# Kernel tuning notes

Measured on AMD Instinct MI355X. Metric: run time of the kernel, lower is better.

The kernel has to match this reference:

```python
import jax, jax.numpy as jnp
import numpy as np


def setup_inputs() -> dict:
    key = jax.random.key(0)
    ks = jax.random.split(key, 5)
    B, C, H, W = 4, 256, 48, 48
    x = jax.random.normal(ks[0], (B, C, H, W), dtype=jnp.float32)
    w_qkv = jax.random.normal(ks[1], (3 * C, C), dtype=jnp.float32) * (C ** -0.5)
    b_qkv = jax.random.normal(ks[2], (3 * C,), dtype=jnp.float32) * 0.02
    w_proj = jax.random.normal(ks[3], (C, C), dtype=jnp.float32) * (C ** -0.5)
    b_proj = jax.random.normal(ks[4], (C,), dtype=jnp.float32) * 0.02
    return {"x": x, "w_qkv": w_qkv, "b_qkv": b_qkv, "w_proj": w_proj, "b_proj": b_proj, "num_heads": 4}


def reference(x, w_qkv, b_qkv, w_proj, b_proj, num_heads):
    B, C, H, W = x.shape
    N = H * W
    hd = C // num_heads
    # NOTE: original uses full-dim scale, not head_dim
    scale = C ** -0.5
    # 1x1 conv == channel matmul
    qkv = jnp.einsum('bchw,oc->bohw', x, w_qkv) + b_qkv[None, :, None, None]
    qkv = qkv.reshape(B, 3, num_heads, hd, N)
    q = qkv[:, 0].transpose(0, 1, 3, 2)  # [B, h, N, d]
    k = qkv[:, 1]                         # [B, h, d, N]
    v = qkv[:, 2].transpose(0, 1, 3, 2)  # [B, h, N, d]
    attn = jax.nn.softmax((q @ k) * scale, axis=-1)  # [B, h, N, N]
    out = attn @ v                        # [B, h, N, d]
    out = out.transpose(0, 1, 3, 2).reshape(B, C, H, W)
    return jnp.einsum('bchw,oc->bohw', out, w_proj) + b_proj[None, :, None, None]
```

## Files before the change

kernel.cpp:

```cpp
#include <hip/hip_runtime.h>
#include <hip/hip_bf16.h>
#include <stdint.h>

typedef unsigned short u16;
typedef unsigned int u32;
typedef __attribute__((ext_vector_type(8))) short bf16x8;
typedef __attribute__((ext_vector_type(4))) float f32x4;
typedef __attribute__((ext_vector_type(4))) unsigned short u16x4;

#define MFMA16 __builtin_amdgcn_mfma_f32_16x16x32_bf16

static constexpr int Bb = 4;
static constexpr int Cc = 256;
static constexpr int NHh = 4;
static constexpr int HDd = 64;
static constexpr int Nn = 2304;

__device__ __forceinline__ u16 f2bf(float f) {
  u32 u = __builtin_bit_cast(u32, f);
  u32 r = u + 0x7fffu + ((u >> 16) & 1u);
  return (u16)(r >> 16);
}

__device__ __forceinline__ u32 cvtpk(float a, float b) {
  u32 r;
  asm("v_cvt_pk_bf16_f32 %0, %1, %2" : "=v"(r) : "v"(a), "v"(b));
  return r;
}

__device__ __forceinline__ void async16(const void* g, void* l) {
  __builtin_amdgcn_global_load_lds(
      (const __attribute__((address_space(1))) u32*)g,
      (__attribute__((address_space(3))) u32*)l, 16, 0, 0);
}

__global__ __launch_bounds__(256) void k_prep(const float* __restrict__ wq,
                                              const float* __restrict__ wp,
                                              const float* __restrict__ x,
                                              u16* __restrict__ wqb,
                                              u16* __restrict__ wpb,
                                              u16* __restrict__ xT) {
  __shared__ float tile[64][65];
  int bx = blockIdx.x;
  if (bx < 768) {
    int i = bx * 256 + threadIdx.x;
    if (i < 3 * Cc * Cc) wqb[i] = f2bf(wq[i]);
    if (i < Cc * Cc)     wpb[i] = f2bf(wp[i]);
    return;
  }
  int t2 = bx - 768;
  int c0 = (t2 & 3) * 64, n0 = ((t2 >> 2) % 36) * 64, b = (t2 >> 2) / 36;
  int w = threadIdx.x >> 6, lane = threadIdx.x & 63;
#pragma unroll
  for (int i = 0; i < 16; ++i) {
    int c = i * 4 + w;
    tile[c][lane] = x[((size_t)(b * Cc + c0 + c)) * Nn + n0 + lane];
  }
  __syncthreads();
#pragma unroll
  for (int i = 0; i < 16; ++i) {
    int n = i * 4 + w;
    xT[((size_t)(b * Nn + n0 + n)) * Cc + c0 + lane] = f2bf(tile[lane][n]);
  }
}

__global__ __launch_bounds__(256) void k_qkv(const u16* __restrict__ wqb,
                                             const u16* __restrict__ xT,
                                             const float* __restrict__ bqkv,
                                             u16* __restrict__ qT, u16* __restrict__ kT,
                                             u16* __restrict__ vT) {
  __shared__ u16 Bs[64 * 256];
  int n0 = blockIdx.y * 64, b = blockIdx.z;
  int t = threadIdx.x, w = t >> 6, l = t & 63, g = l >> 4, li = l & 15;
#pragma unroll
  for (int it = 0; it < 8; ++it) {
    int ch = it * 256 + t;
    int row = ch >> 5, c16 = ch & 31;
    const char* src = (const char*)xT + ((size_t)(b * Nn + n0 + row)) * 512 +
                      ((c16 * 16) ^ ((row & 7) << 4));
    async16(src, (char*)Bs + (it * 256 + (t & ~63)) * 16);
  }
  __syncthreads();
  const float qs = 0.0625f * 1.44269504088896340736f;
#pragma unroll
  for (int p = 0; p < 2; ++p) {
    int o0 = blockIdx.x * 128 + p * 64;
    const u16* Arow = wqb + (size_t)(o0 + w * 16 + li) * Cc;
    f32x4 acc[4] = {};
#pragma unroll
    for (int s = 0; s < 8; ++s) {
      bf16x8 a = *(const bf16x8*)(Arow + s * 32 + g * 8);
#pragma unroll
      for (int nt = 0; nt < 4; ++nt) {
        int row = nt * 16 + li;
        const char* bp_ = (const char*)Bs + row * 512 + ((s * 64 + g * 16) ^ ((row & 7) << 4));
        bf16x8 bb = *(const bf16x8*)bp_;
        acc[nt] = MFMA16(a, bb, acc[nt], 0, 0, 0);
      }
    }
    int which = o0 >> 8;
    int hh = (o0 >> 6) & 3;
    int bh = b * NHh + hh;
    int dbase = w * 16 + g * 4;
#pragma unroll
    for (int nt = 0; nt < 4; ++nt) {
      int n = n0 + nt * 16 + li;
      float v0 = acc[nt][0] + bqkv[o0 + dbase + 0];
      float v1 = acc[nt][1] + bqkv[o0 + dbase + 1];
      float v2 = acc[nt][2] + bqkv[o0 + dbase + 2];
      float v3 = acc[nt][3] + bqkv[o0 + dbase + 3];
      if (which == 0) {
        u16x4 pq = {f2bf(v0 * qs), f2bf(v1 * qs), f2bf(v2 * qs), f2bf(v3 * qs)};
        *(u16x4*)(qT + ((size_t)bh * Nn + n) * HDd + dbase) = pq;
      } else if (which == 1) {
        u16x4 pk = {f2bf(v0), f2bf(v1), f2bf(v2), f2bf(v3)};
        *(u16x4*)(kT + ((size_t)bh * Nn + n) * HDd + dbase) = pk;
      } else {
        vT[((size_t)bh * HDd + dbase + 0) * Nn + n] = f2bf(v0);
        vT[((size_t)bh * HDd + dbase + 1) * Nn + n] = f2bf(v1);
        vT[((size_t)bh * HDd + dbase + 2) * Nn + n] = f2bf(v2);
        vT[((size_t)bh * HDd + dbase + 3) * Nn + n] = f2bf(v3);
      }
    }
  }
}

__global__ __launch_bounds__(192) void k_attn(const u16* __restrict__ qT,
                                              const u16* __restrict__ kT,
                                              const u16* __restrict__ vT,
                                              u16* __restrict__ attP,
                                              float* __restrict__ lsumP) {
  __shared__ u16 Ks[2][32 * 64];
  __shared__ u16 Vs[2][64 * 32];
  __shared__ u16 Ps[3][32 * 32];
  int L = blockIdx.x;
  int xcd = L & 7, r = L >> 3;
  int bh = 2 * xcd + (r >= 96 ? 1 : 0);
  int r2 = (r >= 96) ? r - 96 : r;
  int quarter = r2 / 24;
  int qb = r2 % 24;
  int t = threadIdx.x, w = t / 64, l = t & 63, g = l >> 4, li = l & 15;
  int q0 = qb * 96 + w * 32;
  const u16* qr0 = qT + ((size_t)bh * Nn + q0 + li) * HDd;
  const u16* qr1 = qT + ((size_t)bh * Nn + q0 + 16 + li) * HDd;
  bf16x8 bq[2][2];
  bq[0][0] = *(const bf16x8*)(qr0 + g * 8);
  bq[0][1] = *(const bf16x8*)(qr0 + 32 + g * 8);
  bq[1][0] = *(const bf16x8*)(qr1 + g * 8);
  bq[1][1] = *(const bf16x8*)(qr1 + 32 + g * 8);
  const short one = (short)0x3F80;
  bf16x8 ONES = {one, one, one, one, one, one, one, one};
  f32x4 acc[2][4] = {};
  f32x4 acc_l[2] = {};
  const char* kbh = (const char*)(kT + (size_t)bh * Nn * HDd);
  const char* vbh = (const char*)(vT + (size_t)bh * HDd * Nn);
  char* PsB = (char*)(&Ps[w][0]);
  int sw_li = (li & 7) << 4;
  int sw2   = ((li >> 1) & 3) << 4;

  const char* sp[3];
  int sd[3];
  ptrdiff_t sstr[3];
  bool son[3], svv[3];
#pragma unroll
  for (int it = 0; it < 3; ++it) {
    int gg = w * 3 + it;
    son[it] = (gg < 8);
    int c = gg * 64 + l;
    if (c < 256) {
      int key = c >> 3, c8 = c & 7;
      sp[it] = kbh + (size_t)(quarter * 576 + key) * 128 + ((c8 * 16) ^ ((key & 7) << 4));
      sd[it] = c * 16; sstr[it] = 32 * 128; svv[it] = false;
    } else {
      int cv = c - 256, d = cv >> 2, c4 = cv & 3;
      sp[it] = vbh + (size_t)d * (Nn * 2) + quarter * 1152 +
               ((c4 * 16) ^ (((d >> 1) & 3) << 4));
      sd[it] = cv * 16; sstr[it] = 32 * 2; svv[it] = true;
    }
  }

  auto STAGE = [&](int buf) {
    char* kdst = (char*)(&Ks[0][0]) + buf * 4096;
    char* vdst = (char*)(&Vs[0][0]) + buf * 4096;
#pragma unroll
    for (int it = 0; it < 3; ++it) {
      if (son[it]) {
        async16(sp[it], (svv[it] ? vdst : kdst) + sd[it]);
        sp[it] += sstr[it];
      }
    }
  };

  STAGE(0);
  int cur = 0;
  for (int kb = 0; kb < 18; ++kb) {
    __syncthreads();
    if (kb + 1 < 18) STAGE(cur ^ 1);

    const char* Kc = (const char*)(&Ks[0][0]) + cur * 4096;
    const char* Vc = (const char*)(&Vs[0][0]) + cur * 4096;

    f32x4 s[2][2];
    __builtin_amdgcn_s_setprio(1);
#pragma unroll
    for (int kt = 0; kt < 2; ++kt) {
      const char* kr = Kc + (kt * 16 + li) * 128;
      bf16x8 a0 = *(const bf16x8*)(kr + ((g * 16) ^ sw_li));
      bf16x8 a1 = *(const bf16x8*)(kr + ((64 + g * 16) ^ sw_li));
#pragma unroll
      for (int st = 0; st < 2; ++st) {
        f32x4 z = {};
        z = MFMA16(a0, bq[st][0], z, 0, 0, 0);
        z = MFMA16(a1, bq[st][1], z, 0, 0, 0);
        s[st][kt] = z;
      }
    }
    __builtin_amdgcn_s_setprio(0);

#pragma unroll
    for (int st = 0; st < 2; ++st) {
#pragma unroll
      for (int kt = 0; kt < 2; ++kt)
#pragma unroll
        for (int j = 0; j < 4; ++j) s[st][kt][j] = exp2f(s[st][kt][j]);
      int rq = st * 16 + li;
#pragma unroll
      for (int kt = 0; kt < 2; ++kt) {
        uint2 pk;
        pk.x = cvtpk(s[st][kt][0], s[st][kt][1]);
        pk.y = cvtpk(s[st][kt][2], s[st][kt][3]);
        *(uint2*)(PsB + rq * 64 + ((kt * 32 + g * 8) ^ sw2)) = pk;
      }
    }
    bf16x8 pa[2];
    pa[0] = *(const bf16x8*)(PsB + (0 * 16 + li) * 64 + ((g * 16) ^ sw2));
    pa[1] = *(const bf16x8*)(PsB + (1 * 16 + li) * 64 + ((g * 16) ^ sw2));
    __builtin_amdgcn_s_setprio(1);
    acc_l[0] = MFMA16(pa[0], ONES, acc_l[0], 0, 0, 0);
    acc_l[1] = MFMA16(pa[1], ONES, acc_l[1], 0, 0, 0);
#pragma unroll
    for (int dt = 0; dt < 4; ++dt) {
      const char* vr = Vc + (dt * 16 + li) * 64;
      bf16x8 v0 = *(const bf16x8*)(vr + ((g * 16) ^ sw2));
      acc[0][dt] = MFMA16(pa[0], v0, acc[0][dt], 0, 0, 0);
      acc[1][dt] = MFMA16(pa[1], v0, acc[1][dt], 0, 0, 0);
    }
    __builtin_amdgcn_s_setprio(0);
    cur ^= 1;
  }
  u16* ap = attP + (size_t)quarter * (Bb * Nn * Cc);
  float* lp = lsumP + quarter * (Bb * NHh * Nn);
  if (li == 0) {
#pragma unroll
    for (int st = 0; st < 2; ++st)
#pragma unroll
      for (int j = 0; j < 4; ++j)
        lp[bh * Nn + q0 + st * 16 + g * 4 + j] = acc_l[st][j];
  }
  int b = bh >> 2, hh = bh & 3;
#pragma unroll
  for (int st = 0; st < 2; ++st)
#pragma unroll
    for (int dt = 0; dt < 4; ++dt) {
      int cidx = hh * 64 + dt * 16 + li;
#pragma unroll
      for (int j = 0; j < 4; ++j) {
        ap[((size_t)(b * Nn + q0 + st * 16 + g * 4 + j)) * Cc + cidx] = f2bf(acc[st][dt][j]);
      }
    }
}

__global__ __launch_bounds__(256) void k_proj(const u16* __restrict__ wpb,
                                              const u16* __restrict__ attP,
                                              const float* __restrict__ lsumP,
                                              const float* __restrict__ bp,
                                              float* __restrict__ out) {
  __shared__ u16 Bs[4][32 * 256];
  int bx = blockIdx.x, n0 = blockIdx.y * 32, b = blockIdx.z;
  int t = threadIdx.x, w = t >> 6, l = t & 63, g = l >> 4, li = l & 15;
#pragma unroll
  for (int it = 0; it < 16; ++it) {
    int ch = it * 256 + t;
    int qtr = ch >> 10, rem = ch & 1023;
    int row = rem >> 5, c16 = rem & 31;
    const char* src = (const char*)(attP + (size_t)qtr * (Bb * Nn * Cc)) +
                      ((size_t)(b * Nn + n0 + row)) * 512 +
                      ((c16 * 16) ^ ((row & 7) << 4));
    async16(src, (char*)Bs + (it * 256 + (t & ~63)) * 16);
  }
  const u16* Arow0 = wpb + (size_t)(bx * 128 + w * 16 + li) * Cc;
  const u16* Arow1 = Arow0 + (size_t)64 * Cc;
  __syncthreads();
  f32x4 acc[2][4][2] = {};
#pragma unroll
  for (int s = 0; s < 8; ++s) {
    bf16x8 a0 = *(const bf16x8*)(Arow0 + s * 32 + g * 8);
    bf16x8 a1 = *(const bf16x8*)(Arow1 + s * 32 + g * 8);
#pragma unroll
    for (int qtr = 0; qtr < 4; ++qtr) {
#pragma unroll
      for (int nt = 0; nt < 2; ++nt) {
        int row = nt * 16 + li;
        const char* bp_ = (const char*)Bs + qtr * (32 * 512) + row * 512 +
                          ((s * 64 + g * 16) ^ ((row & 7) << 4));
        bf16x8 bb = *(const bf16x8*)bp_;
        acc[0][s >> 1][nt] = MFMA16(a0, bb, acc[0][s >> 1][nt], 0, 0, 0);
        acc[1][s >> 1][nt] = MFMA16(a1, bb, acc[1][s >> 1][nt], 0, 0, 0);
      }
    }
  }
#pragma unroll
  for (int nt = 0; nt < 2; ++nt) {
    int n = n0 + nt * 16 + li;
    float inv[4];
#pragma unroll
    for (int h = 0; h < 4; ++h) {
      int lidx = (b * NHh + h) * Nn + n;
      float sum = lsumP[lidx] + lsumP[1 * Bb * NHh * Nn + lidx] +
                  lsumP[2 * Bb * NHh * Nn + lidx] + lsumP[3 * Bb * NHh * Nn + lidx];
      inv[h] = 1.0f / sum;
    }
#pragma unroll
    for (int p = 0; p < 2; ++p) {
      int obase = bx * 128 + p * 64 + w * 16 + g * 4;
#pragma unroll
      for (int j = 0; j < 4; ++j) {
        float v = acc[p][0][nt][j] * inv[0] + acc[p][1][nt][j] * inv[1] +
                  acc[p][2][nt][j] * inv[2] + acc[p][3][nt][j] * inv[3];
        out[((size_t)(b * Cc + obase + j)) * Nn + n] = v + bp[obase + j];
      }
    }
  }
}

extern "C" void kernel_launch(void* const* d_in, const int* in_sizes, int n_in,
                              void* d_out, int out_size, void* d_ws, size_t ws_size,
                              hipStream_t stream) {
  const float* x     = (const float*)d_in[0];
  const float* wqkv  = (const float*)d_in[1];
  const float* bqkv  = (const float*)d_in[2];
  const float* wproj = (const float*)d_in[3];
  const float* bproj = (const float*)d_in[4];
  float* out = (float*)d_out;

  u16* ws    = (u16*)d_ws;
  u16* wq_bf = ws;
  u16* wp_bf = wq_bf + 196608;
  u16* qT    = wp_bf + 65536;
  u16* kT    = qT + 2359296;
  u16* vT    = kT + 2359296;
  u16* attP  = vT + 2359296;
  u16* xT    = attP;
  float* lsumP = (float*)(attP + 4 * 2359296);

  k_prep<<<dim3(1344), dim3(256), 0, stream>>>(wqkv, wproj, x, wq_bf, wp_bf, xT);
  k_qkv<<<dim3(6, 36, 4), dim3(256), 0, stream>>>(wq_bf, xT, bqkv, qT, kT, vT);
  k_attn<<<dim3(1536), dim3(192), 0, stream>>>(qT, kT, vT, attP, lsumP);
  k_proj<<<dim3(2, 72, 4), dim3(256), 0, stream>>>(wp_bf, attP, lsumP, bproj, out);
}
```

Measured before the change: 84.31 us.

## Fuse x transpose into QKV kernel and add split-merge kernel before projection

The x transpose/bf16 conversion moves out of the prep kernel into the QKV kernel, which now reads fp32 x directly and transposes it through LDS. This removes the xT round trip through global memory. A new merge kernel sums the four split-K partial attention outputs, normalises them by the combined softmax sums, and writes a single bf16 tensor into the qT buffer. The projection then does a quarter of its previous MFMA work and loads less data into LDS. The cost is an extra kernel launch plus a full read/write pass for the merge, and the QKV kernel now repeats the x transpose in each of its six output-channel blocks.

```diff
diff --git a/kernel.cpp b/kernel.cpp
--- a/kernel.cpp
+++ b/kernel.cpp
@@ -28,6 +28,9 @@
   return r;
 }
 
+__device__ __forceinline__ float blo(u32 u) { return __builtin_bit_cast(float, u << 16); }
+__device__ __forceinline__ float bhi(u32 u) { return __builtin_bit_cast(float, u & 0xffff0000u); }
+
 __device__ __forceinline__ void async16(const void* g, void* l) {
   __builtin_amdgcn_global_load_lds(
       (const __attribute__((address_space(1))) u32*)g,
@@ -36,51 +39,39 @@
 
 __global__ __launch_bounds__(256) void k_prep(const float* __restrict__ wq,
                                               const float* __restrict__ wp,
-                                              const float* __restrict__ x,
                                               u16* __restrict__ wqb,
-                                              u16* __restrict__ wpb,
-                                              u16* __restrict__ xT) {
-  __shared__ float tile[64][65];
-  int bx = blockIdx.x;
-  if (bx < 768) {
-    int i = bx * 256 + threadIdx.x;
-    if (i < 3 * Cc * Cc) wqb[i] = f2bf(wq[i]);
-    if (i < Cc * Cc)     wpb[i] = f2bf(wp[i]);
-    return;
-  }
-  int t2 = bx - 768;
-  int c0 = (t2 & 3) * 64, n0 = ((t2 >> 2) % 36) * 64, b = (t2 >> 2) / 36;
-  int w = threadIdx.x >> 6, lane = threadIdx.x & 63;
-#pragma unroll
-  for (int i = 0; i < 16; ++i) {
-    int c = i * 4 + w;
-    tile[c][lane] = x[((size_t)(b * Cc + c0 + c)) * Nn + n0 + lane];
-  }
-  __syncthreads();
-#pragma unroll
-  for (int i = 0; i < 16; ++i) {
-    int n = i * 4 + w;
-    xT[((size_t)(b * Nn + n0 + n)) * Cc + c0 + lane] = f2bf(tile[lane][n]);
-  }
+                                              u16* __restrict__ wpb) {
+  int i = blockIdx.x * 256 + threadIdx.x;
+  if (i < 3 * Cc * Cc) wqb[i] = f2bf(wq[i]);
+  if (i < Cc * Cc)     wpb[i] = f2bf(wp[i]);
 }
 
 __global__ __launch_bounds__(256) void k_qkv(const u16* __restrict__ wqb,
-                                             const u16* __restrict__ xT,
+                                             const float* __restrict__ x,
                                              const float* __restrict__ bqkv,
                                              u16* __restrict__ qT, u16* __restrict__ kT,
                                              u16* __restrict__ vT) {
+  __shared__ float tile[64][65];
   __shared__ u16 Bs[64 * 256];
   int n0 = blockIdx.y * 64, b = blockIdx.z;
   int t = threadIdx.x, w = t >> 6, l = t & 63, g = l >> 4, li = l & 15;
-#pragma unroll
-  for (int it = 0; it < 8; ++it) {
-    int ch = it * 256 + t;
-    int row = ch >> 5, c16 = ch & 31;
-    const char* src = (const char*)xT + ((size_t)(b * Nn + n0 + row)) * 512 +
-                      ((c16 * 16) ^ ((row & 7) << 4));
-    async16(src, (char*)Bs + (it * 256 + (t & ~63)) * 16);
-  }
-  __syncthreads();
+  char* BsB = (char*)Bs;
+#pragma unroll
+  for (int cc = 0; cc < 4; ++cc) {
+#pragma unroll
+    for (int i = 0; i < 16; ++i) {
+      int cl = i * 4 + w;
+      tile[cl][l] = x[((size_t)(b * Cc + cc * 64 + cl)) * Nn + n0 + l];
+    }
+    __syncthreads();
+#pragma unroll
+    for (int i = 0; i < 16; ++i) {
+      int nr = i * 4 + w;
+      int byte = nr * 512 + ((2 * (cc * 64 + l)) ^ ((nr & 7) << 4));
+      *(u16*)(BsB + byte) = f2bf(tile[l][nr]);
+    }
+    __syncthreads();
+  }
   const float qs = 0.0625f * 1.44269504088896340736f;
 #pragma unroll
   for (int p = 0; p < 2; ++p) {
@@ -270,64 +261,77 @@
     }
 }
 
+__global__ __launch_bounds__(256) void k_merge(const u16* __restrict__ attP,
+                                               const float* __restrict__ lsumP,
+                                               u16* __restrict__ attT) {
+  int gid = blockIdx.x * 256 + threadIdx.x;
+  int base = gid * 8;
+  int bidx = base / (Nn * Cc);
+  int rem = base - bidx * (Nn * Cc);
+  int n = rem >> 8, c = rem & 255;
+  int hh = c >> 6;
+  int lidx = (bidx * NHh + hh) * Nn + n;
+  const int LQ = Bb * NHh * Nn;
+  float inv = 1.0f / (lsumP[lidx] + lsumP[LQ + lidx] +
+                      lsumP[2 * LQ + lidx] + lsumP[3 * LQ + lidx]);
+  const size_t QSZ = (size_t)Bb * Nn * Cc;
+  uint4 p0 = *(const uint4*)(attP + base);
+  uint4 p1 = *(const uint4*)(attP + QSZ + base);
+  uint4 p2 = *(const uint4*)(attP + 2 * QSZ + base);
+  uint4 p3 = *(const uint4*)(attP + 3 * QSZ + base);
+  uint4 o;
+  o.x = cvtpk((blo(p0.x) + blo(p1.x) + blo(p2.x) + blo(p3.x)) * inv,
+              (bhi(p0.x) + bhi(p1.x) + bhi(p2.x) + bhi(p3.x)) * inv);
+  o.y = cvtpk((blo(p0.y) + blo(p1.y) + blo(p2.y) + blo(p3.y)) * inv,
+              (bhi(p0.y) + bhi(p1.y) + bhi(p2.y) + bhi(p3.y)) * inv);
+  o.z = cvtpk((blo(p0.z) + blo(p1.z) + blo(p2.z) + blo(p3.z)) * inv,
+              (bhi(p0.z) + bhi(p1.z) + bhi(p2.z) + bhi(p3.z)) * inv);
+  o.w = cvtpk((blo(p0.w) + blo(p1.w) + blo(p2.w) + blo(p3.w)) * inv,
+              (bhi(p0.w) + bhi(p1.w) + bhi(p2.w) + bhi(p3.w)) * inv);
+  *(uint4*)(attT + base) = o;
+}
+
 __global__ __launch_bounds__(256) void k_proj(const u16* __restrict__ wpb,
-                                              const u16* __restrict__ attP,
-                                              const float* __restrict__ lsumP,
+                                              const u16* __restrict__ attT,
                                               const float* __restrict__ bp,
                                               float* __restrict__ out) {
-  __shared__ u16 Bs[4][32 * 256];
+  __shared__ u16 Bs[32 * 256];
   int bx = blockIdx.x, n0 = blockIdx.y * 32, b = blockIdx.z;
   int t = threadIdx.x, w = t >> 6, l = t & 63, g = l >> 4, li = l & 15;
 #pragma unroll
-  for (int it = 0; it < 16; ++it) {
+  for (int it = 0; it < 4; ++it) {
     int ch = it * 256 + t;
-    int qtr = ch >> 10, rem = ch & 1023;
-    int row = rem >> 5, c16 = rem & 31;
-    const char* src = (const char*)(attP + (size_t)qtr * (Bb * Nn * Cc)) +
-                      ((size_t)(b * Nn + n0 + row)) * 512 +
+    int row = ch >> 5, c16 = ch & 31;
+    const char* src = (const char*)attT + ((size_t)(b * Nn + n0 + row)) * 512 +
                       ((c16 * 16) ^ ((row & 7) << 4));
     async16(src, (char*)Bs + (it * 256 + (t & ~63)) * 16);
   }
   const u16* Arow0 = wpb + (size_t)(bx * 128 + w * 16 + li) * Cc;
   const u16* Arow1 = Arow0 + (size_t)64 * Cc;
   __syncthreads();
-  f32x4 acc[2][4][2] = {};
+  f32x4 acc[2][2] = {};
 #pragma unroll
   for (int s = 0; s < 8; ++s) {
     bf16x8 a0 = *(const bf16x8*)(Arow0 + s * 32 + g * 8);
     bf16x8 a1 = *(const bf16x8*)(Arow1 + s * 32 + g * 8);
 #pragma unroll
-    for (int qtr = 0; qtr < 4; ++qtr) {
-#pragma unroll
-      for (int nt = 0; nt < 2; ++nt) {
-        int row = nt * 16 + li;
-        const char* bp_ = (const char*)Bs + qtr * (32 * 512) + row * 512 +
-                          ((s * 64 + g * 16) ^ ((row & 7) << 4));
-        bf16x8 bb = *(const bf16x8*)bp_;
-        acc[0][s >> 1][nt] = MFMA16(a0, bb, acc[0][s >> 1][nt], 0, 0, 0);
-        acc[1][s >> 1][nt] = MFMA16(a1, bb, acc[1][s >> 1][nt], 0, 0, 0);
-      }
+    for (int nt = 0; nt < 2; ++nt) {
+      int row = nt * 16 + li;
+      const char* bp_ = (const char*)Bs + row * 512 + ((s * 64 + g * 16) ^ ((row & 7) << 4));
+      bf16x8 bb = *(const bf16x8*)bp_;
+      acc[0][nt] = MFMA16(a0, bb, acc[0][nt], 0, 0, 0);
+      acc[1][nt] = MFMA16(a1, bb, acc[1][nt], 0, 0, 0);
     }
   }
 #pragma unroll
   for (int nt = 0; nt < 2; ++nt) {
     int n = n0 + nt * 16 + li;
-    float inv[4];
-#pragma unroll
-    for (int h = 0; h < 4; ++h) {
-      int lidx = (b * NHh + h) * Nn + n;
-      float sum = lsumP[lidx] + lsumP[1 * Bb * NHh * Nn + lidx] +
-                  lsumP[2 * Bb * NHh * Nn + lidx] + lsumP[3 * Bb * NHh * Nn + lidx];
-      inv[h] = 1.0f / sum;
-    }
 #pragma unroll
     for (int p = 0; p < 2; ++p) {
       int obase = bx * 128 + p * 64 + w * 16 + g * 4;
 #pragma unroll
       for (int j = 0; j < 4; ++j) {
-        float v = acc[p][0][nt][j] * inv[0] + acc[p][1][nt][j] * inv[1] +
-                  acc[p][2][nt][j] * inv[2] + acc[p][3][nt][j] * inv[3];
-        out[((size_t)(b * Cc + obase + j)) * Nn + n] = v + bp[obase + j];
+        out[((size_t)(b * Cc + obase + j)) * Nn + n] = acc[p][nt][j] + bp[obase + j];
       }
     }
   }
@@ -350,11 +354,12 @@
   u16* kT    = qT + 2359296;
   u16* vT    = kT + 2359296;
   u16* attP  = vT + 2359296;
-  u16* xT    = attP;
   float* lsumP = (float*)(attP + 4 * 2359296);
-
-  k_prep<<<dim3(1344), dim3(256), 0, stream>>>(wqkv, wproj, x, wq_bf, wp_bf, xT);
-  k_qkv<<<dim3(6, 36, 4), dim3(256), 0, stream>>>(wq_bf, xT, bqkv, qT, kT, vT);
+  u16* attT  = qT;
+
+  k_prep<<<dim3(768), dim3(256), 0, stream>>>(wqkv, wproj, wq_bf, wp_bf);
+  k_qkv<<<dim3(6, 36, 4), dim3(256), 0, stream>>>(wq_bf, x, bqkv, qT, kT, vT);
   k_attn<<<dim3(1536), dim3(192), 0, stream>>>(qT, kT, vT, attP, lsumP);
-  k_proj<<<dim3(2, 72, 4), dim3(256), 0, stream>>>(wp_bf, attP, lsumP, bproj, out);
-}
+  k_merge<<<dim3(1152), dim3(256), 0, stream>>>(attP, lsumP, attT);
+  k_proj<<<dim3(2, 72, 4), dim3(256), 0, stream>>>(wp_bf, attT, bproj, out);
+}
```

Result: slower. 86.82 us (+3.0%).
